# Kernel tuning notes

Hardware: AMD Instinct MI355X
Metric: run time of the kernel (lower is better)

## Reference

```python
import jax, jax.numpy as jnp
import numpy as np

DIM = 256
HEADS = 8
KS = 3          # deform conv kernel size
N = KS * KS     # sampling points per output pixel
PAD = 1


def conv2d(x, w, b=None, stride=1, padding=0):
    out = jax.lax.conv_general_dilated(
        x, w, (stride, stride), [(padding, padding)] * 2,
        dimension_numbers=('NCHW', 'OIHW', 'NCHW'))
    if b is not None:
        out = out + b[None, :, None, None]
    return out


def deform_conv(x, w_pconv, b_pconv, w_dconv):
    b, c, h, w = x.shape
    offset = conv2d(x, w_pconv, b_pconv, padding=1)      # (b, 2N, h, w)
    off = offset.transpose(0, 2, 3, 1)                   # (b, h, w, 2N); [:N]=x-off, [N:]=y-off
    xp = jnp.pad(x, ((0, 0), (0, 0), (PAD, PAD), (PAD, PAD)))
    hp, wp = h + 2 * PAD, w + 2 * PAD
    r = jnp.arange(-(KS - 1) // 2, (KS - 1) // 2 + 1, dtype=x.dtype)
    pnx, pny = jnp.meshgrid(r, r, indexing='ij')
    # sampling positions, 1-indexed into the padded input (matches the torch ref)
    px = off[..., :N] + pnx.reshape(-1) + jnp.arange(1, h + 1, dtype=x.dtype)[None, :, None, None]
    py = off[..., N:] + pny.reshape(-1) + jnp.arange(1, w + 1, dtype=x.dtype)[None, None, :, None]
    fx = jnp.floor(px)
    fy = jnp.floor(py)
    qlt_x = jnp.clip(fx, 0, hp - 1)
    qlt_y = jnp.clip(fy, 0, wp - 1)
    qrb_x = jnp.clip(fx + 1, 0, hp - 1)
    qrb_y = jnp.clip(fy + 1, 0, wp - 1)
    pxc = jnp.clip(px, 0, hp - 1)
    pyc = jnp.clip(py, 0, wp - 1)
    # bilinear weights (can be negative at clamped borders, as in the torch ref)
    g_lt = (1 + (qlt_x - pxc)) * (1 + (qlt_y - pyc))
    g_rb = (1 - (qrb_x - pxc)) * (1 - (qrb_y - pyc))
    g_lb = (1 + (qlt_x - pxc)) * (1 - (qrb_y - pyc))
    g_rt = (1 - (qrb_x - pxc)) * (1 + (qlt_y - pyc))
    ilt_x = qlt_x.astype(jnp.int32)
    ilt_y = qlt_y.astype(jnp.int32)
    irb_x = qrb_x.astype(jnp.int32)
    irb_y = qrb_y.astype(jnp.int32)

    def gather(xb, ix, iy):
        return xb[:, ix, iy]                              # (c, h, w, N)

    gat = jax.vmap(gather)
    x_lt = gat(xp, ilt_x, ilt_y)
    x_rb = gat(xp, irb_x, irb_y)
    x_lb = gat(xp, ilt_x, irb_y)
    x_rt = gat(xp, irb_x, ilt_y)
    x_off = (g_lt[:, None] * x_lt + g_rb[:, None] * x_rb
             + g_lb[:, None] * x_lb + g_rt[:, None] * x_rt)   # (b, c, h, w, N)
    # 'b c h w (i j) -> b c (h i) (w j)' then ks-strided conv
    x_off = x_off.reshape(b, c, h, w, KS, KS).transpose(0, 1, 2, 4, 3, 5)
    x_off = x_off.reshape(b, c, h * KS, w * KS)
    return conv2d(x_off, w_dconv, None, stride=KS)


def ssa_forward(x, w_pconv, b_pconv, w_dconv, w_qkv, temperature, w_proj):
    b, c, h, w = x.shape
    hw = h * w
    ch = c // HEADS
    q = deform_conv(x, w_pconv, b_pconv, w_dconv)         # (b, c, h, w)
    qkv = jnp.einsum('bchw,oc->bohw', x, w_qkv)           # 1x1 conv, (b, 3c, h, w)
    k = qkv[:, c:2 * c]
    v = qkv[:, 2 * c:]
    q = q.reshape(b, HEADS, ch, hw)
    k = k.reshape(b, HEADS, ch, hw)
    v = v.reshape(b, HEADS, ch, hw)
    k = k / jnp.maximum(jnp.linalg.norm(k, axis=-1, keepdims=True), 1e-12)
    v = v / jnp.maximum(jnp.linalg.norm(v, axis=-1, keepdims=True), 1e-12)
    attn = jnp.einsum('bhcn,bhdn->bhcd', q, k) * temperature[None]   # (b, h, ch, ch)
    attn = jax.nn.softmax(attn, axis=-1)
    out = jnp.einsum('bhcd,bhdn->bhcn', attn, v).reshape(b, c, h, w)
    return jnp.einsum('bchw,oc->bohw', out, w_proj)       # project_out 1x1


def setup_inputs() -> dict:
    key = jax.random.key(0)
    ks = jax.random.split(key, 6)
    B, H, W = 2, 96, 96
    x = jax.random.normal(ks[0], (B, DIM, H, W), jnp.float32)
    w_pconv = jax.random.normal(ks[1], (2 * N, DIM, KS, KS), jnp.float32) * 0.01
    b_pconv = jax.random.normal(ks[2], (2 * N,), jnp.float32) * 0.01
    w_dconv = jax.random.normal(ks[3], (DIM, DIM, KS, KS), jnp.float32) * 0.02
    w_qkv = jax.random.normal(ks[4], (3 * DIM, DIM), jnp.float32) * 0.05
    temperature = jnp.ones((HEADS, 1, 1), jnp.float32)
    w_proj = jax.random.normal(ks[5], (DIM, DIM), jnp.float32) * 0.05
    return dict(x=x, w_pconv=w_pconv, b_pconv=b_pconv, w_dconv=w_dconv,
                w_qkv=w_qkv, temperature=temperature, w_proj=w_proj)


def reference(x, w_pconv, b_pconv, w_dconv, w_qkv, temperature, w_proj):
    return ssa_forward(x, w_pconv, b_pconv, w_dconv, w_qkv, temperature, w_proj)
```

## Files before the change

### kernel.cpp

```cpp
#include <hip/hip_runtime.h>
#include <math.h>

#define BB 2
#define CC 256
#define HW 96
#define PP 9216
#define KO 18
#define HEADS 8
#define NCH 18

typedef short bf16x8 __attribute__((ext_vector_type(8)));
typedef float f32x4 __attribute__((ext_vector_type(4)));

#define NP_O    0UL
#define W2_O    147456UL
#define IDX_O   331776UL
#define WGT_O   995328UL
#define WT2_O   1658880UL
#define WP2_O   2248704UL
#define WQ2_O   2322432UL
#define QP_O    2584576UL
#define KV_O    12021760UL
#define INV_O   21458944UL
#define AP_O    21459968UL
#define V2T_O   331776UL

__device__ __forceinline__ ushort f2bf_rne(float f) {
    unsigned u = __float_as_uint(f);
    unsigned r = (u + 0x7FFFu + ((u >> 16) & 1u)) >> 16;
    return (ushort)r;
}
__device__ __forceinline__ float bf2f(ushort h) {
    return __uint_as_float(((unsigned)h) << 16);
}

__global__ __launch_bounds__(256) void k_prep_wt(const float* __restrict__ wd,
                                                 ushort* __restrict__ h,
                                                 ushort* __restrict__ lo) {
    int tid = blockIdx.x * 256 + threadIdx.x;
    if (tid >= 9 * 8 * 1024 * 8) return;
    int e = tid & 7;
    int u = (tid >> 3) & 1023;
    int cs = (tid >> 13) & 7;
    int kk = tid >> 16;
    int oh = u >> 6, rem = u & 63;
    int lrow = rem & 15, lhi = rem >> 4;
    int o = oh * 16 + lrow;
    int c = cs * 32 + lhi * 8 + e;
    float v = wd[o * 2304 + c * 9 + kk];
    ushort hh = f2bf_rne(v);
    h[tid] = hh;
    lo[tid] = f2bf_rne(v - bf2f(hh));
}

__global__ __launch_bounds__(256) void k_prep_wp(const float* __restrict__ wp,
                                                 ushort* __restrict__ h,
                                                 ushort* __restrict__ lo) {
    int tid = blockIdx.x * 256 + threadIdx.x;
    if (tid >= 9 * 8 * 128 * 8) return;
    int e = tid & 7;
    int u = (tid >> 3) & 127;
    int cs = (tid >> 10) & 7;
    int kk = tid >> 13;
    int mf = u >> 6, rem = u & 63;
    int lrow = rem & 15, lhi = rem >> 4;
    int o = mf * 16 + lrow;
    int c = cs * 32 + lhi * 8 + e;
    float v = (o < KO) ? wp[(o * 256 + c) * 9 + kk] : 0.f;
    ushort hh = f2bf_rne(v);
    h[tid] = hh;
    lo[tid] = f2bf_rne(v - bf2f(hh));
}

__global__ __launch_bounds__(256) void k_prep_w(const float* __restrict__ W,
                                                ushort* __restrict__ h,
                                                ushort* __restrict__ lo,
                                                int total) {
    int tid = blockIdx.x * 256 + threadIdx.x;
    if (tid >= total) return;
    int e = tid & 7;
    int u = (tid >> 3) & 1023;
    int csg = (tid >> 13) & 7;
    int mt = tid >> 16;
    int rem = u & 63;
    int lrow = rem & 15, lhi = rem >> 4;
    int o = mt * 256 + (u >> 6) * 16 + lrow;
    int c = csg * 32 + lhi * 8 + e;
    float v = W[o * 256 + c];
    ushort hh = f2bf_rne(v);
    h[tid] = hh;
    lo[tid] = f2bf_rne(v - bf2f(hh));
}

__global__ __launch_bounds__(256) void k_pconv(const float* __restrict__ x,
                                               const ushort* __restrict__ wp2h,
                                               const ushort* __restrict__ wp2l,
                                               float* __restrict__ ppart) {
    int s = blockIdx.x;
    int xcd = s & 7;
    int b = xcd & 1, ks = xcd >> 1;
    int p0 = (s >> 3) * 64;
    int t = threadIdx.x;
    int l = t & 63, w = t >> 6;
    int lrow = l & 15, lhi = l >> 4;
    int p = t & 63, cg = t >> 6;
    __shared__ __align__(16) ushort Sh[64 * 40];
    __shared__ __align__(16) ushort Sl[64 * 40];
    f32x4 acc[2];
    acc[0] = (f32x4)0.f; acc[1] = (f32x4)0.f;
    const float* xb = x + (size_t)b * CC * PP;
    int pix = p0 + p;
    int i_ = pix / 96, j_ = pix % 96;
#pragma unroll 1
    for (int cs = 0; cs < 2; ++cs) {
        int csg = ks * 2 + cs;
        const float* xc0 = xb + (size_t)(csg * 32 + cg * 8) * PP;
#pragma unroll 1
        for (int kk = 0; kk < 9; ++kk) {
            int di = kk / 3 - 1, dj = kk % 3 - 1;
            bool vOK = ((unsigned)(i_ + di) < 96u) && ((unsigned)(j_ + dj) < 96u);
            int poff = pix + di * 96 + dj;
            __syncthreads();
            bf16x8 ah[2], al[2];
#pragma unroll
            for (int mf = 0; mf < 2; ++mf) {
                size_t gi = (((size_t)(kk * 8 + csg)) * 128 + (mf * 64 + l)) * 8;
                ah[mf] = *(const bf16x8*)&wp2h[gi];
                al[mf] = *(const bf16x8*)&wp2l[gi];
            }
            bf16x8 vh, vl;
#pragma unroll
            for (int i = 0; i < 8; ++i) {
                float v = vOK ? xc0[(size_t)i * PP + poff] : 0.f;
                ushort hh = f2bf_rne(v);
                vh[i] = (short)hh;
                vl[i] = (short)f2bf_rne(v - bf2f(hh));
            }
            *(bf16x8*)&Sh[p * 40 + cg * 8] = vh;
            *(bf16x8*)&Sl[p * 40 + cg * 8] = vl;
            __syncthreads();
            bf16x8 Bh = *(const bf16x8*)&Sh[(w * 16 + lrow) * 40 + lhi * 8];
            bf16x8 Bl = *(const bf16x8*)&Sl[(w * 16 + lrow) * 40 + lhi * 8];
#pragma unroll
            for (int mf = 0; mf < 2; ++mf) {
                acc[mf] = __builtin_amdgcn_mfma_f32_16x16x32_bf16(ah[mf], Bh, acc[mf], 0, 0, 0);
                acc[mf] = __builtin_amdgcn_mfma_f32_16x16x32_bf16(ah[mf], Bl, acc[mf], 0, 0, 0);
                acc[mf] = __builtin_amdgcn_mfma_f32_16x16x32_bf16(al[mf], Bh, acc[mf], 0, 0, 0);
            }
        }
    }
    float* pr = ppart + ((size_t)(ks * BB + b) * 32) * PP;
#pragma unroll
    for (int mf = 0; mf < 2; ++mf)
#pragma unroll
        for (int j = 0; j < 4; ++j)
            pr[(size_t)(mf * 16 + lhi * 4 + j) * PP + p0 + w * 16 + lrow] = acc[mf][j];
}

__global__ __launch_bounds__(256) void k_bilin2(const float* __restrict__ pp,
                                                const float* __restrict__ bp,
                                                int4* __restrict__ idx4,
                                                float4* __restrict__ wgt4) {
    int idx = blockIdx.x * 256 + threadIdx.x;
    if (idx >= BB * 9 * PP) return;
    int p = idx % PP;
    int bn = idx / PP;
    int n = bn % 9, b = bn / 9;
    int i = p / 96, j = p % 96;
    float ox = bp[n], oy = bp[n + 9];
#pragma unroll
    for (int k = 0; k < 4; ++k) {
        ox += pp[((size_t)(k * BB + b) * 32 + n) * PP + p];
        oy += pp[((size_t)(k * BB + b) * 32 + n + 9) * PP + p];
    }
    float px = ox + (float)(n / 3 - 1) + (float)(i + 1);
    float py = oy + (float)(n % 3 - 1) + (float)(j + 1);
    float fx = floorf(px), fy = floorf(py);
    float qltx = fminf(fmaxf(fx, 0.f), 97.f);
    float qlty = fminf(fmaxf(fy, 0.f), 97.f);
    float qrbx = fminf(fmaxf(fx + 1.f, 0.f), 97.f);
    float qrby = fminf(fmaxf(fy + 1.f, 0.f), 97.f);
    float pxc = fminf(fmaxf(px, 0.f), 97.f);
    float pyc = fminf(fmaxf(py, 0.f), 97.f);
    float glt = (1.f + (qltx - pxc)) * (1.f + (qlty - pyc));
    float grb = (1.f - (qrbx - pxc)) * (1.f - (qrby - pyc));
    float glb = (1.f + (qltx - pxc)) * (1.f - (qrby - pyc));
    float grt = (1.f - (qrbx - pxc)) * (1.f + (qlty - pyc));
    int x0 = (int)qltx - 1, y0 = (int)qlty - 1;
    int x1 = (int)qrbx - 1, y1 = (int)qrby - 1;
    bool vlt = (x0 >= 0 && x0 < 96 && y0 >= 0 && y0 < 96);
    bool vrb = (x1 >= 0 && x1 < 96 && y1 >= 0 && y1 < 96);
    bool vlb = (x0 >= 0 && x0 < 96 && y1 >= 0 && y1 < 96);
    bool vrt = (x1 >= 0 && x1 < 96 && y0 >= 0 && y0 < 96);
    int4 id;
    id.x = vlt ? x0 * 96 + y0 : 0;
    id.y = vrb ? x1 * 96 + y1 : 0;
    id.z = vlb ? x0 * 96 + y1 : 0;
    id.w = vrt ? x1 * 96 + y0 : 0;
    idx4[idx] = id;
    wgt4[idx] = make_float4(vlt ? glt : 0.f, vrb ? grb : 0.f,
                            vlb ? glb : 0.f, vrt ? grt : 0.f);
}

__global__ __launch_bounds__(256) void k_dconv(const float* __restrict__ x,
                                               const ushort* __restrict__ wt2h,
                                               const ushort* __restrict__ wt2l,
                                               const int4* __restrict__ idx4,
                                               const float4* __restrict__ wgt4,
                                               float* __restrict__ qpart) {
    int s = blockIdx.x;
    int xcd = s & 7, ib = s >> 3;
    int combo = xcd >> 1;
    int b = combo & 1;
    int half = combo >> 1;
    int ptile = (xcd & 1) * 144 + ib;
    int p0 = ptile * 32;
    int t = threadIdx.x;
    int l = t & 63, w = t >> 6;
    int lrow = l & 15, lhi = l >> 4;
    int obase = w * 64;
    int pl = t & 31, cg = t >> 5;

    __shared__ __align__(16) ushort Sh0[32 * 40], Sl0[32 * 40];
    __shared__ __align__(16) ushort Sh1[32 * 40], Sl1[32 * 40];
    __shared__ int4 Tid[9 * 32];
    __shared__ float4 Twg[9 * 32];

    for (int e = t; e < 9 * 32; e += 256) {
        int kk = e >> 5, pq = e & 31;
        size_t tb = ((size_t)b * 9 + kk) * PP + p0 + pq;
        Tid[e] = idx4[tb];
        Twg[e] = wgt4[tb];
    }

    f32x4 acc[4][2];
#pragma unroll
    for (int mf = 0; mf < 4; ++mf)
#pragma unroll
        for (int nf = 0; nf < 2; ++nf) acc[mf][nf] = (f32x4)0.f;

    const float* xb = x + (size_t)b * CC * PP;
    int h4 = half * 4;

    float R[16];
    float4 g4r;

    auto LD = [&](int i) {
        int cs = i / 9, kk = i % 9;
        int csg = h4 + cs;
        int4 id = Tid[kk * 32 + pl];
        g4r = Twg[kk * 32 + pl];
        const float* xp0 = xb + (size_t)(csg * 32 + cg * 4) * PP;
#pragma unroll
        for (int q = 0; q < 4; ++q) {
            const float* xc = xp0 + (size_t)q * PP;
            R[q * 4 + 0] = xc[id.x];
            R[q * 4 + 1] = xc[id.y];
            R[q * 4 + 2] = xc[id.z];
            R[q * 4 + 3] = xc[id.w];
        }
    };
    auto CONV = [&](ushort* Sh, ushort* Sl) {
        ushort4 vh, vl;
#pragma unroll
        for (int q = 0; q < 4; ++q) {
            float v = g4r.x * R[q * 4 + 0];
            v = fmaf(g4r.y, R[q * 4 + 1], v);
            v = fmaf(g4r.z, R[q * 4 + 2], v);
            v = fmaf(g4r.w, R[q * 4 + 3], v);
            ushort hh = f2bf_rne(v);
            ushort ll = f2bf_rne(v - bf2f(hh));
            if (q == 0)      { vh.x = hh; vl.x = ll; }
            else if (q == 1) { vh.y = hh; vl.y = ll; }
            else if (q == 2) { vh.z = hh; vl.z = ll; }
            else             { vh.w = hh; vl.w = ll; }
        }
        *(ushort4*)&Sh[pl * 40 + cg * 4] = vh;
        *(ushort4*)&Sl[pl * 40 + cg * 4] = vl;
    };
    auto COMPUTE = [&](int i, const ushort* Sh, const ushort* Sl) {
        int cs = i / 9, kk = i % 9;
        int csg = h4 + cs;
        bf16x8 ah[4], al[4];
#pragma unroll
        for (int mf = 0; mf < 4; ++mf) {
            size_t gi = (((size_t)(kk * 8 + csg)) * 1024 + ((w * 4 + mf) * 64 + l)) * 8;
            ah[mf] = *(const bf16x8*)&wt2h[gi];
            al[mf] = *(const bf16x8*)&wt2l[gi];
        }
        bf16x8 Bh2[2], Bl2[2];
#pragma unroll
        for (int nf = 0; nf < 2; ++nf) {
            Bh2[nf] = *(const bf16x8*)&Sh[(nf * 16 + lrow) * 40 + lhi * 8];
            Bl2[nf] = *(const bf16x8*)&Sl[(nf * 16 + lrow) * 40 + lhi * 8];
        }
        __builtin_amdgcn_s_setprio(1);
#pragma unroll
        for (int mf = 0; mf < 4; ++mf)
#pragma unroll
            for (int nf = 0; nf < 2; ++nf) {
                acc[mf][nf] = __builtin_amdgcn_mfma_f32_16x16x32_bf16(ah[mf], Bh2[nf], acc[mf][nf], 0, 0, 0);
                acc[mf][nf] = __builtin_amdgcn_mfma_f32_16x16x32_bf16(ah[mf], Bl2[nf], acc[mf][nf], 0, 0, 0);
                acc[mf][nf] = __builtin_amdgcn_mfma_f32_16x16x32_bf16(al[mf], Bh2[nf], acc[mf][nf], 0, 0, 0);
            }
        __builtin_amdgcn_s_setprio(0);
    };

    __syncthreads();
    LD(0); CONV(Sh0, Sl0);
    LD(1);
    __syncthreads();

#pragma unroll 1
    for (int i0 = 0; i0 < 36; i0 += 2) {
        CONV(Sh1, Sl1);
        if (i0 + 2 < 36) LD(i0 + 2);
        COMPUTE(i0, Sh0, Sl0);
        __syncthreads();
        if (i0 + 2 < 36) CONV(Sh0, Sl0);
        if (i0 + 3 < 36) LD(i0 + 3);
        COMPUTE(i0 + 1, Sh1, Sl1);
        __syncthreads();
    }

    float* qh = qpart + (size_t)half * BB * CC * PP + (size_t)b * CC * PP;
#pragma unroll
    for (int mf = 0; mf < 4; ++mf)
#pragma unroll
        for (int nf = 0; nf < 2; ++nf)
#pragma unroll
            for (int j = 0; j < 4; ++j)
                qh[(size_t)(obase + mf * 16 + lhi * 4 + j) * PP + p0 + nf * 16 + lrow] =
                    acc[mf][nf][j];
}

__global__ __launch_bounds__(256) void k_gemm_bf(const float* __restrict__ Bsrc,
                                                 const ushort* __restrict__ B2h,
                                                 const ushort* __restrict__ B2l,
                                                 const ushort* __restrict__ A2h,
                                                 const ushort* __restrict__ A2l,
                                                 float* __restrict__ C,
                                                 int mtiles, int bRowStride, int bRowOff,
                                                 int aBatchStride,
                                                 float* __restrict__ npart) {
    int s = blockIdx.x;
    int xcd = s & 7, ib = s >> 3;
    int b, mt, ptile;
    if (mtiles == 2) {
        int combo = xcd >> 1;
        b = combo & 1; mt = combo >> 1;
        ptile = (xcd & 1) * 72 + ib;
    } else {
        b = xcd >> 2; mt = 0;
        ptile = (xcd & 3) * 36 + ib;
    }
    int p0 = ptile * 64;
    int t = threadIdx.x;
    int l = t & 63, w = t >> 6;
    int lrow = l & 15, lhi = l >> 4;
    int obase = w * 64;
    int p = t & 63, cg = t >> 6;
    __shared__ __align__(16) ushort Sh[64 * 40];
    __shared__ __align__(16) ushort Sl[64 * 40];
    f32x4 acc[4][4];
#pragma unroll
    for (int mf = 0; mf < 4; ++mf)
#pragma unroll
        for (int nf = 0; nf < 4; ++nf) acc[mf][nf] = (f32x4)0.f;
    const ushort* Ah = A2h + (size_t)b * aBatchStride;
    const ushort* Al = A2l + (size_t)b * aBatchStride;
#pragma unroll 1
    for (int csg = 0; csg < 8; ++csg) {
        __syncthreads();
        bf16x8 ah[4], al[4];
#pragma unroll
        for (int mf = 0; mf < 4; ++mf) {
            size_t gi = (((size_t)(mt * 8 + csg)) * 1024 + ((w * 4 + mf) * 64 + l)) * 8;
            ah[mf] = *(const bf16x8*)&Ah[gi];
            al[mf] = *(const bf16x8*)&Al[gi];
        }
        if (B2h) {
            size_t bo = ((((size_t)b * 144 + ptile) * 8 + csg) * 4 + cg) * 512 + (size_t)p * 8;
            bf16x8 vh = *(const bf16x8*)&B2h[bo];
            bf16x8 vl = *(const bf16x8*)&B2l[bo];
            *(bf16x8*)&Sh[p * 40 + cg * 8] = vh;
            *(bf16x8*)&Sl[p * 40 + cg * 8] = vl;
        } else {
            const float* Bb = Bsrc + ((size_t)b * bRowStride + bRowOff) * PP;
            const float* xr = Bb + (size_t)(csg * 32 + cg * 8) * PP + p0 + p;
            bf16x8 vh, vl;
#pragma unroll
            for (int i = 0; i < 8; ++i) {
                float v = xr[(size_t)i * PP];
                ushort hh = f2bf_rne(v);
                vh[i] = (short)hh;
                vl[i] = (short)f2bf_rne(v - bf2f(hh));
            }
            *(bf16x8*)&Sh[p * 40 + cg * 8] = vh;
            *(bf16x8*)&Sl[p * 40 + cg * 8] = vl;
        }
        __syncthreads();
        bf16x8 Bh4[4], Bl4[4];
#pragma unroll
        for (int nf = 0; nf < 4; ++nf) {
            Bh4[nf] = *(const bf16x8*)&Sh[(nf * 16 + lrow) * 40 + lhi * 8];
            Bl4[nf] = *(const bf16x8*)&Sl[(nf * 16 + lrow) * 40 + lhi * 8];
        }
#pragma unroll
        for (int mf = 0; mf < 4; ++mf) {
#pragma unroll
            for (int nf = 0; nf < 4; ++nf) {
                acc[mf][nf] = __builtin_amdgcn_mfma_f32_16x16x32_bf16(ah[mf], Bh4[nf], acc[mf][nf], 0, 0, 0);
                acc[mf][nf] = __builtin_amdgcn_mfma_f32_16x16x32_bf16(ah[mf], Bl4[nf], acc[mf][nf], 0, 0, 0);
                acc[mf][nf] = __builtin_amdgcn_mfma_f32_16x16x32_bf16(al[mf], Bh4[nf], acc[mf][nf], 0, 0, 0);
            }
        }
    }
    float* Cb = C + (size_t)b * (mtiles * 256) * PP;
#pragma unroll
    for (int mf = 0; mf < 4; ++mf)
#pragma unroll
        for (int nf = 0; nf < 4; ++nf)
#pragma unroll
            for (int j = 0; j < 4; ++j)
                Cb[(size_t)(mt * 256 + obase + mf * 16 + lhi * 4 + j) * PP + p0 + nf * 16 + lrow] =
                    acc[mf][nf][j];
    if (npart) {
        float sq[4][4];
#pragma unroll
        for (int mf = 0; mf < 4; ++mf)
#pragma unroll
            for (int j = 0; j < 4; ++j) {
                float v0 = acc[mf][0][j], v1 = acc[mf][1][j];
                float v2 = acc[mf][2][j], v3 = acc[mf][3][j];
                sq[mf][j] = v0 * v0 + v1 * v1 + v2 * v2 + v3 * v3;
            }
#pragma unroll
        for (int m = 1; m <= 8; m <<= 1)
#pragma unroll
            for (int mf = 0; mf < 4; ++mf)
#pragma unroll
                for (int j = 0; j < 4; ++j)
                    sq[mf][j] += __shfl_xor(sq[mf][j], m, 64);
        if (lrow == 0) {
            float* np = npart + ((size_t)(b * 2 + mt) * 144 + ptile) * 256;
#pragma unroll
            for (int mf = 0; mf < 4; ++mf)
#pragma unroll
                for (int j = 0; j < 4; ++j)
                    np[obase + mf * 16 + lhi * 4 + j] = sq[mf][j];
        }
    }
}

__global__ __launch_bounds__(256) void k_prep_v(const float* __restrict__ kv,
                                                ushort* __restrict__ v2h,
                                                ushort* __restrict__ v2l) {
    int s = blockIdx.x;
    int b = s / 1152;
    int r = s % 1152;
    int pt = r >> 3, csg = r & 7;
    int t = threadIdx.x;
    __shared__ float T[32][65];
    const float* src = kv + ((size_t)b * 512 + 256 + csg * 32) * PP + pt * 64;
    {
        int c = t >> 3, p8 = (t & 7) * 8;
        const float* row = src + (size_t)c * PP + p8;
        float4 a = *(const float4*)&row[0];
        float4 d = *(const float4*)&row[4];
        T[c][p8 + 0] = a.x; T[c][p8 + 1] = a.y; T[c][p8 + 2] = a.z; T[c][p8 + 3] = a.w;
        T[c][p8 + 4] = d.x; T[c][p8 + 5] = d.y; T[c][p8 + 6] = d.z; T[c][p8 + 7] = d.w;
    }
    __syncthreads();
    int cc = t >> 6, pl = t & 63;
    bf16x8 vh, vl;
#pragma unroll
    for (int e = 0; e < 8; ++e) {
        float v = T[cc * 8 + e][pl];
        ushort hh = f2bf_rne(v);
        vh[e] = (short)hh;
        vl[e] = (short)f2bf_rne(v - bf2f(hh));
    }
    size_t o = ((((size_t)b * 144 + pt) * 8 + csg) * 4 + cc) * 512 + (size_t)pl * 8;
    *(bf16x8*)&v2h[o] = vh;
    *(bf16x8*)&v2l[o] = vl;
}

__global__ __launch_bounds__(256) void k_attn_part(const float* __restrict__ qp,
                                                   const float* __restrict__ kv,
                                                   float* __restrict__ apart) {
    int ch = blockIdx.x, h = blockIdx.y, b = blockIdx.z;
    int t = threadIdx.x;
    int d = t & 31, cg = t >> 5;
    __shared__ float qs[32][37], ks[32][37];
    float acc[4] = {0.f, 0.f, 0.f, 0.f};
    const float* q0 = qp + ((size_t)b * CC + h * 32) * PP;
    const float* q1 = q0 + (size_t)BB * CC * PP;
    const float* kb = kv + ((size_t)b * 512 + h * 32) * PP;
    int r = t >> 3, cq = (t & 7) * 4;
    for (int po = ch * 512; po < ch * 512 + 512; po += 32) {
        float4 va = *(const float4*)&q0[(size_t)r * PP + po + cq];
        float4 vb = *(const float4*)&q1[(size_t)r * PP + po + cq];
        qs[r][cq + 0] = va.x + vb.x; qs[r][cq + 1] = va.y + vb.y;
        qs[r][cq + 2] = va.z + vb.z; qs[r][cq + 3] = va.w + vb.w;
        float4 vk = *(const float4*)&kb[(size_t)r * PP + po + cq];
        ks[r][cq + 0] = vk.x; ks[r][cq + 1] = vk.y;
        ks[r][cq + 2] = vk.z; ks[r][cq + 3] = vk.w;
        __syncthreads();
#pragma unroll
        for (int pq = 0; pq < 32; ++pq) {
            float kvv = ks[d][pq];
#pragma unroll
            for (int i = 0; i < 4; ++i)
                acc[i] = fmaf(qs[cg * 4 + i][pq], kvv, acc[i]);
        }
        __syncthreads();
    }
    float* ap = apart + (((size_t)(b * 8 + h) * NCH + ch) << 10);
#pragma unroll
    for (int i = 0; i < 4; ++i) ap[(cg * 4 + i) * 32 + d] = acc[i];
}

__global__ __launch_bounds__(256) void k_attn_fin_w2(const float* __restrict__ apart,
                                                     const float* __restrict__ npart,
                                                     const float* __restrict__ temp,
                                                     const float* __restrict__ wproj,
                                                     ushort* __restrict__ w2h,
                                                     ushort* __restrict__ w2l) {
    int h = blockIdx.x, b = blockIdx.y;
    int t = threadIdx.x;
    __shared__ float A[32][33];
    __shared__ float invk[32], invv[32];
    if (t < 64) {
        int mt = t >> 5, row = (t & 31) + h * 32;
        const float* base = npart + ((size_t)(b * 2 + mt) * 144) * 256 + row;
        float ssum = 0.f;
        for (int pt = 0; pt < 144; ++pt) ssum += base[pt * 256];
        float iv = 1.f / fmaxf(sqrtf(ssum), 1e-12f);
        if (mt == 0) invk[t & 31] = iv; else invv[t & 31] = iv;
    }
    const float* ap = apart + ((size_t)(b * 8 + h) * NCH << 10);
    float th = temp[h];
    for (int e = t; e < 1024; e += 256) {
        float s = 0.f;
        for (int chn = 0; chn < NCH; ++chn) s += ap[chn * 1024 + e];
        A[e >> 5][e & 31] = s * th;
    }
    __syncthreads();
    if (t < 32) {
        int c = t;
        float m = -INFINITY;
        float row[32];
#pragma unroll
        for (int d = 0; d < 32; ++d) {
            row[d] = A[c][d] * invk[d];
            m = fmaxf(m, row[d]);
        }
        float sum = 0.f;
#pragma unroll
        for (int d = 0; d < 32; ++d) sum += expf(row[d] - m);
        float inv = 1.f / sum;
#pragma unroll
        for (int d = 0; d < 32; ++d)
            A[c][d] = expf(row[d] - m) * inv * invv[d];
    }
    __syncthreads();
    int o = t;
    float wrow[32];
#pragma unroll
    for (int c = 0; c < 32; ++c) wrow[c] = wproj[o * 256 + h * 32 + c];
    int wq = o >> 6, mf = (o >> 4) & 3, lr = o & 15;
    size_t bb = (size_t)b * 65536;
#pragma unroll
    for (int e = 0; e < 32; ++e) {
        float v = 0.f;
#pragma unroll
        for (int c = 0; c < 32; ++c) v = fmaf(wrow[c], A[c][e], v);
        int lhi = e >> 3, ee = e & 7;
        size_t gi = bb + ((size_t)h * 1024 + ((wq * 4 + mf) * 64 + lhi * 16 + lr)) * 8 + ee;
        ushort hh = f2bf_rne(v);
        w2h[gi] = hh;
        w2l[gi] = f2bf_rne(v - bf2f(hh));
    }
}

extern "C" void kernel_launch(void* const* d_in, const int* in_sizes, int n_in,
                              void* d_out, int out_size, void* d_ws, size_t ws_size,
                              hipStream_t stream) {
    const float* x     = (const float*)d_in[0];
    const float* wp    = (const float*)d_in[1];
    const float* bp    = (const float*)d_in[2];
    const float* wd    = (const float*)d_in[3];
    const float* wqkv  = (const float*)d_in[4];
    const float* temp  = (const float*)d_in[5];
    const float* wproj = (const float*)d_in[6];
    float* out = (float*)d_out;
    float* ws  = (float*)d_ws;

    float* npart  = ws + NP_O;
    ushort* w2h   = (ushort*)(ws + W2_O);
    ushort* w2l   = w2h + 2 * 65536;
    int4*  idx4   = (int4*)(ws + IDX_O);
    float4* wgt4  = (float4*)(ws + WGT_O);
    ushort* wt2h  = (ushort*)(ws + WT2_O);
    ushort* wt2l  = wt2h + 9 * 8 * 1024 * 8;
    ushort* wp2h  = (ushort*)(ws + WP2_O);
    ushort* wp2l  = wp2h + 9 * 8 * 128 * 8;
    ushort* wq2h  = (ushort*)(ws + WQ2_O);
    ushort* wq2l  = wq2h + 2 * 8 * 1024 * 8;
    float* qpart  = ws + QP_O;
    float* ppart  = ws + QP_O;
    float* kv     = ws + KV_O;
    float* apart  = ws + AP_O;
    ushort* v2th  = (ushort*)(ws + V2T_O);
    ushort* v2tl  = v2th + 4718592;

    k_prep_wt<<<2304, 256, 0, stream>>>(wd, wt2h, wt2l);
    k_prep_wp<<<288, 256, 0, stream>>>(wp, wp2h, wp2l);
    k_prep_w<<<512, 256, 0, stream>>>(wqkv + 256 * 256, wq2h, wq2l, 2 * 65536);
    k_pconv<<<1152, 256, 0, stream>>>(x, wp2h, wp2l, ppart);
    k_bilin2<<<(BB * 9 * PP + 255) / 256, 256, 0, stream>>>(ppart, bp, idx4, wgt4);
    k_dconv<<<1152, 256, 0, stream>>>(x, wt2h, wt2l, idx4, wgt4, qpart);
    k_gemm_bf<<<576, 256, 0, stream>>>(x, nullptr, nullptr, wq2h, wq2l, kv,
                                       2, 256, 0, 0, npart);
    k_attn_part<<<dim3(NCH, HEADS, BB), 256, 0, stream>>>(qpart, kv, apart);
    k_attn_fin_w2<<<dim3(HEADS, BB), 256, 0, stream>>>(apart, npart, temp, wproj, w2h, w2l);
    k_prep_v<<<2304, 256, 0, stream>>>(kv, v2th, v2tl);
    k_gemm_bf<<<288, 256, 0, stream>>>(nullptr, v2th, v2tl, w2h, w2l, out,
                                       1, 0, 0, 65536, nullptr);
}
```

Measured before the change: 304.3 us.

## Restructure deform conv GEMM to per-wave pixel tiles without shared memory

The deformable conv kernel now gives each wave 16 pixels against all 256 output channels, so each lane builds its own MFMA B operand straight from gathered registers. Shared-memory staging, index tables and barriers are removed, and the block tile grows to 64 pixels with half as many blocks. The cost is much higher register pressure (64 accumulator floats plus two 32-float gather buffers), which can lower occupancy. Each wave also reloads all A-weight fragments from global memory, so weight traffic per pixel goes up.

```diff
diff --git a/kernel.cpp b/kernel.cpp
--- a/kernel.cpp
+++ b/kernel.cpp
@@ -21,7 +21,6 @@
 #define WQ2_O   2322432UL
 #define QP_O    2584576UL
 #define KV_O    12021760UL
-#define INV_O   21458944UL
 #define AP_O    21459968UL
 #define V2T_O   331776UL
 
@@ -213,125 +212,90 @@
     int combo = xcd >> 1;
     int b = combo & 1;
     int half = combo >> 1;
-    int ptile = (xcd & 1) * 144 + ib;
-    int p0 = ptile * 32;
+    int ptile = (xcd & 1) * 72 + ib;
+    int p0 = ptile * 64;
     int t = threadIdx.x;
-    int l = t & 63, w = t >> 6;
+    int w = t >> 6, l = t & 63;
     int lrow = l & 15, lhi = l >> 4;
-    int obase = w * 64;
-    int pl = t & 31, cg = t >> 5;
-
-    __shared__ __align__(16) ushort Sh0[32 * 40], Sl0[32 * 40];
-    __shared__ __align__(16) ushort Sh1[32 * 40], Sl1[32 * 40];
-    __shared__ int4 Tid[9 * 32];
-    __shared__ float4 Twg[9 * 32];
-
-    for (int e = t; e < 9 * 32; e += 256) {
-        int kk = e >> 5, pq = e & 31;
-        size_t tb = ((size_t)b * 9 + kk) * PP + p0 + pq;
-        Tid[e] = idx4[tb];
-        Twg[e] = wgt4[tb];
-    }
-
-    f32x4 acc[4][2];
-#pragma unroll
-    for (int mf = 0; mf < 4; ++mf)
-#pragma unroll
-        for (int nf = 0; nf < 2; ++nf) acc[mf][nf] = (f32x4)0.f;
+    int mypix = p0 + w * 16 + lrow;
 
     const float* xb = x + (size_t)b * CC * PP;
     int h4 = half * 4;
 
-    float R[16];
-    float4 g4r;
-
-    auto LD = [&](int i) {
+    f32x4 acc[16];
+#pragma unroll
+    for (int mf = 0; mf < 16; ++mf) acc[mf] = (f32x4)0.f;
+
+    float R0[32], R1[32];
+    float4 g0, g1;
+
+    auto LD = [&](int i, float (&R)[32], float4& g) {
         int cs = i / 9, kk = i % 9;
         int csg = h4 + cs;
-        int4 id = Tid[kk * 32 + pl];
-        g4r = Twg[kk * 32 + pl];
-        const float* xp0 = xb + (size_t)(csg * 32 + cg * 4) * PP;
-#pragma unroll
-        for (int q = 0; q < 4; ++q) {
-            const float* xc = xp0 + (size_t)q * PP;
-            R[q * 4 + 0] = xc[id.x];
-            R[q * 4 + 1] = xc[id.y];
-            R[q * 4 + 2] = xc[id.z];
-            R[q * 4 + 3] = xc[id.w];
+        size_t tb = ((size_t)b * 9 + kk) * PP + mypix;
+        int4 id = idx4[tb];
+        g = wgt4[tb];
+        const float* xc0 = xb + (size_t)(csg * 32 + lhi * 8) * PP;
+#pragma unroll
+        for (int e = 0; e < 8; ++e) {
+            const float* xc = xc0 + (size_t)e * PP;
+            R[e * 4 + 0] = xc[id.x];
+            R[e * 4 + 1] = xc[id.y];
+            R[e * 4 + 2] = xc[id.z];
+            R[e * 4 + 3] = xc[id.w];
         }
     };
-    auto CONV = [&](ushort* Sh, ushort* Sl) {
-        ushort4 vh, vl;
-#pragma unroll
-        for (int q = 0; q < 4; ++q) {
-            float v = g4r.x * R[q * 4 + 0];
-            v = fmaf(g4r.y, R[q * 4 + 1], v);
-            v = fmaf(g4r.z, R[q * 4 + 2], v);
-            v = fmaf(g4r.w, R[q * 4 + 3], v);
+    auto CONV = [&](const float (&R)[32], float4 g, bf16x8& bh, bf16x8& bl) {
+#pragma unroll
+        for (int e = 0; e < 8; ++e) {
+            float v = g.x * R[e * 4 + 0];
+            v = fmaf(g.y, R[e * 4 + 1], v);
+            v = fmaf(g.z, R[e * 4 + 2], v);
+            v = fmaf(g.w, R[e * 4 + 3], v);
             ushort hh = f2bf_rne(v);
-            ushort ll = f2bf_rne(v - bf2f(hh));
-            if (q == 0)      { vh.x = hh; vl.x = ll; }
-            else if (q == 1) { vh.y = hh; vl.y = ll; }
-            else if (q == 2) { vh.z = hh; vl.z = ll; }
-            else             { vh.w = hh; vl.w = ll; }
-        }
-        *(ushort4*)&Sh[pl * 40 + cg * 4] = vh;
-        *(ushort4*)&Sl[pl * 40 + cg * 4] = vl;
+            bh[e] = (short)hh;
+            bl[e] = (short)f2bf_rne(v - bf2f(hh));
+        }
     };
-    auto COMPUTE = [&](int i, const ushort* Sh, const ushort* Sl) {
+    auto MM = [&](int i, bf16x8 bh, bf16x8 bl) {
         int cs = i / 9, kk = i % 9;
         int csg = h4 + cs;
-        bf16x8 ah[4], al[4];
-#pragma unroll
-        for (int mf = 0; mf < 4; ++mf) {
-            size_t gi = (((size_t)(kk * 8 + csg)) * 1024 + ((w * 4 + mf) * 64 + l)) * 8;
-            ah[mf] = *(const bf16x8*)&wt2h[gi];
-            al[mf] = *(const bf16x8*)&wt2l[gi];
-        }
-        bf16x8 Bh2[2], Bl2[2];
-#pragma unroll
-        for (int nf = 0; nf < 2; ++nf) {
-            Bh2[nf] = *(const bf16x8*)&Sh[(nf * 16 + lrow) * 40 + lhi * 8];
-            Bl2[nf] = *(const bf16x8*)&Sl[(nf * 16 + lrow) * 40 + lhi * 8];
-        }
-        __builtin_amdgcn_s_setprio(1);
-#pragma unroll
-        for (int mf = 0; mf < 4; ++mf)
-#pragma unroll
-            for (int nf = 0; nf < 2; ++nf) {
-                acc[mf][nf] = __builtin_amdgcn_mfma_f32_16x16x32_bf16(ah[mf], Bh2[nf], acc[mf][nf], 0, 0, 0);
-                acc[mf][nf] = __builtin_amdgcn_mfma_f32_16x16x32_bf16(ah[mf], Bl2[nf], acc[mf][nf], 0, 0, 0);
-                acc[mf][nf] = __builtin_amdgcn_mfma_f32_16x16x32_bf16(al[mf], Bh2[nf], acc[mf][nf], 0, 0, 0);
-            }
-        __builtin_amdgcn_s_setprio(0);
+        const ushort* ah0 = wt2h + ((size_t)(kk * 8 + csg)) * 8192;
+        const ushort* al0 = wt2l + ((size_t)(kk * 8 + csg)) * 8192;
+#pragma unroll
+        for (int mf = 0; mf < 16; ++mf) {
+            bf16x8 ah = *(const bf16x8*)&ah0[(size_t)(mf * 64 + l) * 8];
+            bf16x8 al = *(const bf16x8*)&al0[(size_t)(mf * 64 + l) * 8];
+            acc[mf] = __builtin_amdgcn_mfma_f32_16x16x32_bf16(ah, bh, acc[mf], 0, 0, 0);
+            acc[mf] = __builtin_amdgcn_mfma_f32_16x16x32_bf16(ah, bl, acc[mf], 0, 0, 0);
+            acc[mf] = __builtin_amdgcn_mfma_f32_16x16x32_bf16(al, bh, acc[mf], 0, 0, 0);
+        }
     };
 
-    __syncthreads();
-    LD(0); CONV(Sh0, Sl0);
-    LD(1);
-    __syncthreads();
-
+    LD(0, R0, g0);
+    LD(1, R1, g1);
 #pragma unroll 1
     for (int i0 = 0; i0 < 36; i0 += 2) {
-        CONV(Sh1, Sl1);
-        if (i0 + 2 < 36) LD(i0 + 2);
-        COMPUTE(i0, Sh0, Sl0);
-        __syncthreads();
-        if (i0 + 2 < 36) CONV(Sh0, Sl0);
-        if (i0 + 3 < 36) LD(i0 + 3);
-        COMPUTE(i0 + 1, Sh1, Sl1);
-        __syncthreads();
+        {
+            bf16x8 bh, bl;
+            CONV(R0, g0, bh, bl);
+            if (i0 + 2 < 36) LD(i0 + 2, R0, g0);
+            MM(i0, bh, bl);
+        }
+        {
+            bf16x8 bh, bl;
+            CONV(R1, g1, bh, bl);
+            if (i0 + 3 < 36) LD(i0 + 3, R1, g1);
+            MM(i0 + 1, bh, bl);
+        }
     }
 
     float* qh = qpart + (size_t)half * BB * CC * PP + (size_t)b * CC * PP;
 #pragma unroll
-    for (int mf = 0; mf < 4; ++mf)
-#pragma unroll
-        for (int nf = 0; nf < 2; ++nf)
-#pragma unroll
-            for (int j = 0; j < 4; ++j)
-                qh[(size_t)(obase + mf * 16 + lhi * 4 + j) * PP + p0 + nf * 16 + lrow] =
-                    acc[mf][nf][j];
+    for (int mf = 0; mf < 16; ++mf)
+#pragma unroll
+        for (int j = 0; j < 4; ++j)
+            qh[(size_t)(mf * 16 + lhi * 4 + j) * PP + mypix] = acc[mf][j];
 }
 
 __global__ __launch_bounds__(256) void k_gemm_bf(const float* __restrict__ Bsrc,
@@ -620,7 +584,7 @@
     k_prep_w<<<512, 256, 0, stream>>>(wqkv + 256 * 256, wq2h, wq2l, 2 * 65536);
     k_pconv<<<1152, 256, 0, stream>>>(x, wp2h, wp2l, ppart);
     k_bilin2<<<(BB * 9 * PP + 255) / 256, 256, 0, stream>>>(ppart, bp, idx4, wgt4);
-    k_dconv<<<1152, 256, 0, stream>>>(x, wt2h, wt2l, idx4, wgt4, qpart);
+    k_dconv<<<576, 256, 0, stream>>>(x, wt2h, wt2l, idx4, wgt4, qpart);
     k_gemm_bf<<<576, 256, 0, stream>>>(x, nullptr, nullptr, wq2h, wq2l, kv,
                                        2, 256, 0, 0, npart);
     k_attn_part<<<dim3(NCH, HEADS, BB), 256, 0, stream>>>(qpart, kv, apart);
```

After: 861.4 us. 2.83x slower.
